# Performance work log

Measured on AMD Instinct MI355X. Metric: run time of the kernel, lower is better.

The kernel has to match this reference:

```python
import jax, jax.numpy as jnp
import numpy as np

N_NODES = 50000
N_EDGES = 600000
D_IN = 128
D_HID = 128
D_OUT = 64


def setup_inputs() -> dict:
    key = jax.random.key(0)
    ks = jax.random.split(key, 8)
    x = jax.random.normal(ks[0], (N_NODES, D_IN), dtype=jnp.float32)
    edge_index = jax.random.randint(ks[1], (2, N_EDGES), 0, N_NODES, dtype=jnp.int32)
    s = 0.05
    W1l = jax.random.normal(ks[2], (D_HID, D_IN), dtype=jnp.float32) * s
    b1 = jnp.zeros((D_HID,), dtype=jnp.float32)
    W1r = jax.random.normal(ks[3], (D_HID, D_IN), dtype=jnp.float32) * s
    W2l = jax.random.normal(ks[4], (D_OUT, D_HID), dtype=jnp.float32) * s
    b2 = jnp.zeros((D_OUT,), dtype=jnp.float32)
    W2r = jax.random.normal(ks[5], (D_OUT, D_HID), dtype=jnp.float32) * s
    return {"x": x, "edge_index": edge_index, "W1l": W1l, "b1": b1,
            "W1r": W1r, "W2l": W2l, "b2": b2, "W2r": W2r}


def _sage_conv(x, src, dst, Wl, bl, Wr, n_nodes):
    # mean aggregation of source features at destination nodes
    msg_sum = jax.ops.segment_sum(x[src], dst, num_segments=n_nodes)  # [N, D]
    deg = jax.ops.segment_sum(jnp.ones((src.shape[0], 1), x.dtype), dst,
                              num_segments=n_nodes)                   # [N, 1]
    mean = msg_sum / jnp.maximum(deg, 1.0)
    # out = lin_l(mean_neighbors) + lin_r(x_self); bias only on lin_l (PyG default)
    return mean @ Wl.T + bl + x @ Wr.T


def reference(x, edge_index, W1l, b1, W1r, W2l, b2, W2r):
    src, dst = edge_index[0], edge_index[1]
    n = x.shape[0]
    h = jax.nn.relu(_sage_conv(x, src, dst, W1l, b1, W1r, n))
    # dropout p=0.5 is identity in eval mode (training=False)
    return _sage_conv(h, src, dst, W2l, b2, W2r, n)
```

## Files before the change

kernel.cpp:

```cpp
#include <hip/hip_runtime.h>
#include <hip/hip_bf16.h>

typedef __bf16 bf16x8 __attribute__((ext_vector_type(8)));
typedef float f32x4 __attribute__((ext_vector_type(4)));
typedef float f32x2 __attribute__((ext_vector_type(2)));

#define D_FEAT 128
#define CHUNK 1024
#define NW 49344

__device__ __forceinline__ float bits_to_f(unsigned int u) {
    union { unsigned int i; float f; } c; c.i = u; return c.f;
}
__device__ __forceinline__ unsigned short f_to_bf16(float f) {
    __hip_bfloat16 h = (__hip_bfloat16)f;
    return *(unsigned short*)&h;
}
__device__ __forceinline__ float ld(const void* p, int is16, size_t i) {
    return is16 ? (float)((const __hip_bfloat16*)p)[i] : ((const float*)p)[i];
}
__device__ __forceinline__ unsigned int pack4_fp8(float v0, float v1, float v2, float v3) {
    int w = __builtin_amdgcn_cvt_pk_fp8_f32(v0, v1, 0, false);
    w = __builtin_amdgcn_cvt_pk_fp8_f32(v2, v3, w, true);
    return (unsigned int)w;
}
__device__ __forceinline__ int wave_probe16(const void* p) {
    const unsigned short v = ((const unsigned short*)p)[(threadIdx.x & 63) * 2];
    int e = (v >> 7) & 0xFF;
    unsigned long long m = __ballot(e >= 100 && e <= 140);
    return (__popcll(m) >= 48) ? 1 : 0;
}

__global__ void setup_kernel(const void* x,
                             const void* W1l, const void* b1, const void* W1r,
                             const void* W2l, const void* b2, const void* W2r,
                             const int* __restrict__ dst, int E,
                             unsigned short* __restrict__ wout, int* __restrict__ deg) {
    int i = blockIdx.x * blockDim.x + threadIdx.x;
    if (i < NW) {
        int is16 = wave_probe16(x);
        const void* s; int base;
        if      (i < 16384) { s = W1l; base = 0; }
        else if (i < 32768) { s = W1r; base = 16384; }
        else if (i < 40960) { s = W2l; base = 32768; }
        else if (i < 49152) { s = W2r; base = 40960; }
        else if (i < 49280) { s = b1;  base = 49152; }
        else                { s = b2;  base = 49280; }
        wout[i] = f_to_bf16(ld(s, is16, i - base));
    } else {
        int j = i - NW;
        if (j < E) atomicAdd(&deg[dst[j]], 1);
    }
}

__global__ void scan1_kernel(const int* __restrict__ deg, int* __restrict__ bsum, int n) {
    __shared__ int ws[4];
    const int lane = threadIdx.x & 63, wv = threadIdx.x >> 6;
    int i0 = blockIdx.x * CHUNK + threadIdx.x * 4;
    int s = 0;
    #pragma unroll
    for (int j = 0; j < 4; ++j)
        if (i0 + j < n) { int d = deg[i0 + j]; s += (d + 3) & ~3; }
    #pragma unroll
    for (int d = 1; d < 64; d <<= 1) s += __shfl_xor(s, d, 64);
    if (lane == 0) ws[wv] = s;
    __syncthreads();
    if (threadIdx.x == 0) bsum[blockIdx.x] = ws[0] + ws[1] + ws[2] + ws[3];
}

__global__ void scan3_kernel(const int* __restrict__ deg, const int* __restrict__ bsum,
                             int nb, int* __restrict__ off, int* __restrict__ cursor,
                             int* __restrict__ esrc, int n) {
    __shared__ int ws[4];
    const int lane = threadIdx.x & 63, wv = threadIdx.x >> 6;
    int bv = (lane < nb) ? bsum[lane] : 0;
    int bsc = bv;
    #pragma unroll
    for (int s = 1; s < 64; s <<= 1) {
        int t = __shfl_up(bsc, s, 64);
        if (lane >= s) bsc += t;
    }
    const int base = __shfl(bsc, blockIdx.x, 64) - __shfl(bv, blockIdx.x, 64);
    const int total = __shfl(bsc, nb - 1, 64);

    int i0 = blockIdx.x * CHUNK + threadIdx.x * 4;
    int d0 = 0, d1 = 0, d2 = 0, d3 = 0;
    if (i0 + 0 < n) d0 = deg[i0 + 0];
    if (i0 + 1 < n) d1 = deg[i0 + 1];
    if (i0 + 2 < n) d2 = deg[i0 + 2];
    if (i0 + 3 < n) d3 = deg[i0 + 3];
    int v0 = (d0 + 3) & ~3, v1 = (d1 + 3) & ~3, v2 = (d2 + 3) & ~3, v3 = (d3 + 3) & ~3;
    int tsum = v0 + v1 + v2 + v3;
    int sc = tsum;
    #pragma unroll
    for (int s = 1; s < 64; s <<= 1) {
        int t = __shfl_up(sc, s, 64);
        if (lane >= s) sc += t;
    }
    if (lane == 63) ws[wv] = sc;
    __syncthreads();
    int woff = 0;
    for (int w = 0; w < wv; ++w) woff += ws[w];
    int p = base + woff + (sc - tsum);
    #define EMIT(idx, dj, vj)                                            \
        if (i0 + idx < n) {                                              \
            off[i0 + idx] = p; cursor[i0 + idx] = p;                     \
            for (int q = p + dj; q < p + vj; ++q) esrc[q] = n;           \
            p += vj;                                                     \
        }
    EMIT(0, d0, v0) EMIT(1, d1, v1) EMIT(2, d2, v2) EMIT(3, d3, v3)
    #undef EMIT
    if (blockIdx.x == 0 && threadIdx.x == 0) off[n] = total;
}

__global__ void fill_kernel(const int* __restrict__ src, const int* __restrict__ dst,
                            int* __restrict__ cursor, int* __restrict__ esrc, int E) {
    int i = blockIdx.x * blockDim.x + threadIdx.x;
    if (i < E) {
        int p = atomicAdd(&cursor[dst[i]], 1);
        esrc[p] = src[i];
    }
}

template <int NOUT, bool PROBE_A, bool ZA_FP8>
__global__ __launch_bounds__(256)
void gemm_dual_kernel(const void* __restrict__ A,
                      const unsigned short* __restrict__ Wa,
                      const unsigned short* __restrict__ Wb,
                      const unsigned short* __restrict__ bias,
                      void* __restrict__ za, unsigned short* __restrict__ zb,
                      unsigned int* __restrict__ zrow, int zrow_words, int N) {
    if (blockIdx.x == 0 && threadIdx.x < zrow_words) zrow[threadIdx.x] = 0;
    int a16 = 1;
    if (PROBE_A) a16 = wave_probe16(A);

    const int lane = threadIdx.x & 63;
    const int wave = threadIdx.x >> 6;
    const int sel = wave & 1;
    const int m0 = blockIdx.x * 64 + (wave >> 1) * 32;
    if (m0 >= N) return;
    const int lrow = lane & 15;
    const int kg = lane >> 4;
    const unsigned short* W = sel ? Wb : Wa;
    constexpr int NT = NOUT / 16;

    bf16x8 xf[2][4];
    #pragma unroll
    for (int rt = 0; rt < 2; ++rt) {
        const int gr = min(m0 + rt * 16 + lrow, N - 1);
        #pragma unroll
        for (int ks = 0; ks < 4; ++ks) {
            const int k0 = ks * 32 + kg * 8;
            if (a16) {
                xf[rt][ks] = *(const bf16x8*)((const unsigned short*)A + (size_t)gr * D_FEAT + k0);
            } else {
                const float* fp = (const float*)A + (size_t)gr * D_FEAT + k0;
                float4 f0 = *(const float4*)fp, f1 = *(const float4*)(fp + 4);
                union { bf16x8 v; unsigned short us[8]; } t;
                t.us[0] = f_to_bf16(f0.x); t.us[1] = f_to_bf16(f0.y);
                t.us[2] = f_to_bf16(f0.z); t.us[3] = f_to_bf16(f0.w);
                t.us[4] = f_to_bf16(f1.x); t.us[5] = f_to_bf16(f1.y);
                t.us[6] = f_to_bf16(f1.z); t.us[7] = f_to_bf16(f1.w);
                xf[rt][ks] = t.v;
            }
        }
    }

    f32x4 acc[2][NT];
    #pragma unroll
    for (int rt = 0; rt < 2; ++rt)
        #pragma unroll
        for (int t = 0; t < NT; ++t) acc[rt][t] = (f32x4){0, 0, 0, 0};

    #pragma unroll
    for (int ks = 0; ks < 4; ++ks) {
        const int k0 = ks * 32 + kg * 8;
        #pragma unroll
        for (int t = 0; t < NT; ++t) {
            bf16x8 wf = *(const bf16x8*)(W + (size_t)(t * 16 + lrow) * D_FEAT + k0);
            acc[0][t] = __builtin_amdgcn_mfma_f32_16x16x32_bf16(wf, xf[0][ks], acc[0][t], 0, 0, 0);
            acc[1][t] = __builtin_amdgcn_mfma_f32_16x16x32_bf16(wf, xf[1][ks], acc[1][t], 0, 0, 0);
        }
    }

    #pragma unroll
    for (int rt = 0; rt < 2; ++rt) {
        const int nd = m0 + rt * 16 + lrow;
        if (nd < N) {
            #pragma unroll
            for (int t = 0; t < NT; ++t) {
                const int c0 = t * 16 + kg * 4;
                float v0 = acc[rt][t][0], v1 = acc[rt][t][1];
                float v2 = acc[rt][t][2], v3 = acc[rt][t][3];
                if (sel) {
                    uint2 bb = *(const uint2*)(bias + c0);
                    v0 += bits_to_f(bb.x << 16); v1 += bits_to_f(bb.x & 0xffff0000u);
                    v2 += bits_to_f(bb.y << 16); v3 += bits_to_f(bb.y & 0xffff0000u);
                    unsigned int p0 = (unsigned int)f_to_bf16(v0) | ((unsigned int)f_to_bf16(v1) << 16);
                    unsigned int p1 = (unsigned int)f_to_bf16(v2) | ((unsigned int)f_to_bf16(v3) << 16);
                    *(uint2*)(zb + (size_t)nd * NOUT + c0) = make_uint2(p0, p1);
                } else if (ZA_FP8) {
                    *(unsigned int*)((unsigned char*)za + (size_t)nd * NOUT + c0) =
                        pack4_fp8(v0, v1, v2, v3);
                } else {
                    unsigned int p0 = (unsigned int)f_to_bf16(v0) | ((unsigned int)f_to_bf16(v1) << 16);
                    unsigned int p1 = (unsigned int)f_to_bf16(v2) | ((unsigned int)f_to_bf16(v3) << 16);
                    *(uint2*)((unsigned short*)za + (size_t)nd * NOUT + c0) = make_uint2(p0, p1);
                }
            }
        }
    }
}

__global__ __launch_bounds__(256)
void agg1_kernel(const unsigned char* __restrict__ zl,
                 unsigned short* __restrict__ h,
                 const int* __restrict__ off, const int* __restrict__ deg,
                 const int* __restrict__ esrc, int N) {
    const int lane = threadIdx.x & 63;
    const int wave = threadIdx.x >> 6;
    const int a_lo = (blockIdx.x * 4 + wave) * 4;
    if (a_lo >= N) return;
    const int a_hi = min(a_lo + 4, N);
    const int nn = a_hi - a_lo;
    int offv = off[min(a_lo + min(lane, 4), N)];
    int degv = deg[min(a_lo + min(lane, 3), N - 1)];
    #define OFFAT(i) __shfl(offv, (i), 64)
    const int e_beg = OFFAT(0);
    const int e_end = OFFAT(nn);
    const int quarter = lane >> 4;
    const int fl = lane & 15;
    float ax[8];
    #pragma unroll
    for (int i = 0; i < 8; ++i) ax[i] = 0.f;
    int g = a_lo;
    int gend = OFFAT(1);

    auto flush = [&](int gg) {
        int td = __shfl(degv, gg - a_lo, 64);
        float inv = 1.f / (float)(td > 0 ? td : 1);
        float v[8];
        #pragma unroll
        for (int i = 0; i < 8; ++i) {
            float s = ax[i];
            s += __shfl_xor(s, 16, 64); s += __shfl_xor(s, 32, 64);
            v[i] = s * inv; ax[i] = 0.f;
        }
        if (quarter == 0) {
            unsigned short* hp = h + (size_t)gg * D_FEAT + fl * 8;
            uint4 zr = *(const uint4*)hp;
            unsigned int w[4] = {zr.x, zr.y, zr.z, zr.w};
            unsigned int pk[4];
            #pragma unroll
            for (int i = 0; i < 4; ++i) {
                float r0 = fmaxf(v[2 * i]     + bits_to_f(w[i] << 16), 0.f);
                float r1 = fmaxf(v[2 * i + 1] + bits_to_f(w[i] & 0xffff0000u), 0.f);
                pk[i] = (unsigned int)f_to_bf16(r0) | ((unsigned int)f_to_bf16(r1) << 16);
            }
            *(uint4*)hp = make_uint4(pk[0], pk[1], pk[2], pk[3]);
        }
    };

    int cur = (e_beg < e_end) ? esrc[min(e_beg + (lane & 31), e_end - 1)] : 0;
    for (int e = e_beg; e < e_end; e += 32) {
        int nxt = (e + 32 < e_end) ? esrc[min(e + 32 + (lane & 31), e_end - 1)] : 0;
        uint2 r[8];
        #pragma unroll
        for (int k = 0; k < 8; ++k) {
            int sk = __shfl(cur, 4 * k + quarter, 64);
            r[k] = *(const uint2*)(zl + (size_t)sk * D_FEAT + fl * 8);
        }
        #pragma unroll
        for (int k = 0; k < 8; ++k) {
            const int eb = e + 4 * k;
            if (eb < e_end) {
                while (eb >= gend) {
                    flush(g); ++g;
                    gend = OFFAT(min(g - a_lo + 1, 4));
                }
                f32x2 p0 = __builtin_amdgcn_cvt_pk_f32_fp8((int)r[k].x, false);
                f32x2 p1 = __builtin_amdgcn_cvt_pk_f32_fp8((int)r[k].x, true);
                f32x2 p2 = __builtin_amdgcn_cvt_pk_f32_fp8((int)r[k].y, false);
                f32x2 p3 = __builtin_amdgcn_cvt_pk_f32_fp8((int)r[k].y, true);
                ax[0] += p0.x; ax[1] += p0.y; ax[2] += p1.x; ax[3] += p1.y;
                ax[4] += p2.x; ax[5] += p2.y; ax[6] += p3.x; ax[7] += p3.y;
            }
        }
        cur = nxt;
    }
    while (g < a_hi) {
        flush(g); ++g;
        gend = OFFAT(min(g - a_lo + 1, 4));
    }
    #undef OFFAT
}

__global__ __launch_bounds__(256)
void agg2_kernel(const unsigned short* __restrict__ z2l,
                 const unsigned short* __restrict__ s2,
                 void* __restrict__ out, const void* __restrict__ x,
                 const int* __restrict__ off, const int* __restrict__ deg,
                 const int* __restrict__ esrc, int N) {
    const int o16 = wave_probe16(x);
    const int lane = threadIdx.x & 63;
    const int wave = threadIdx.x >> 6;
    const int a_lo = (blockIdx.x * 4 + wave) * 4;
    if (a_lo >= N) return;
    const int a_hi = min(a_lo + 4, N);
    const int nn = a_hi - a_lo;
    int offv = off[min(a_lo + min(lane, 4), N)];
    int degv = deg[min(a_lo + min(lane, 3), N - 1)];
    #define OFFAT(i) __shfl(offv, (i), 64)
    const int e_beg = OFFAT(0);
    const int e_end = OFFAT(nn);
    const int quarter = lane >> 4;
    const int fl = lane & 15;
    float ax[4];
    #pragma unroll
    for (int i = 0; i < 4; ++i) ax[i] = 0.f;
    int g = a_lo;
    int gend = OFFAT(1);

    auto flush = [&](int gg) {
        int td = __shfl(degv, gg - a_lo, 64);
        float inv = 1.f / (float)(td > 0 ? td : 1);
        float v[4];
        #pragma unroll
        for (int i = 0; i < 4; ++i) {
            float s = ax[i];
            s += __shfl_xor(s, 16, 64); s += __shfl_xor(s, 32, 64);
            v[i] = s * inv; ax[i] = 0.f;
        }
        if (quarter == 0) {
            uint2 sb = *(const uint2*)(s2 + (size_t)gg * 64 + fl * 4);
            v[0] += bits_to_f(sb.x << 16); v[1] += bits_to_f(sb.x & 0xffff0000u);
            v[2] += bits_to_f(sb.y << 16); v[3] += bits_to_f(sb.y & 0xffff0000u);
            if (o16) {
                unsigned int p0 = (unsigned int)f_to_bf16(v[0]) | ((unsigned int)f_to_bf16(v[1]) << 16);
                unsigned int p1 = (unsigned int)f_to_bf16(v[2]) | ((unsigned int)f_to_bf16(v[3]) << 16);
                *(uint2*)((unsigned short*)out + (size_t)gg * 64 + fl * 4) = make_uint2(p0, p1);
            } else {
                *(float4*)((float*)out + (size_t)gg * 64 + fl * 4) =
                    make_float4(v[0], v[1], v[2], v[3]);
            }
        }
    };

    int cur = (e_beg < e_end) ? esrc[min(e_beg + (lane & 31), e_end - 1)] : 0;
    for (int e = e_beg; e < e_end; e += 32) {
        int nxt = (e + 32 < e_end) ? esrc[min(e + 32 + (lane & 31), e_end - 1)] : 0;
        uint2 r[8];
        #pragma unroll
        for (int k = 0; k < 8; ++k) {
            int sk = __shfl(cur, 4 * k + quarter, 64);
            r[k] = *(const uint2*)(z2l + (size_t)sk * 64 + fl * 4);
        }
        #pragma unroll
        for (int k = 0; k < 8; ++k) {
            const int eb = e + 4 * k;
            if (eb < e_end) {
                while (eb >= gend) {
                    flush(g); ++g;
                    gend = OFFAT(min(g - a_lo + 1, 4));
                }
                uint2 u = r[k];
                ax[0] += bits_to_f(u.x << 16); ax[1] += bits_to_f(u.x & 0xffff0000u);
                ax[2] += bits_to_f(u.y << 16); ax[3] += bits_to_f(u.y & 0xffff0000u);
            }
        }
        cur = nxt;
    }
    while (g < a_hi) {
        flush(g); ++g;
        gend = OFFAT(min(g - a_lo + 1, 4));
    }
    #undef OFFAT
}

extern "C" void kernel_launch(void* const* d_in, const int* in_sizes, int n_in,
                              void* d_out, int out_size, void* d_ws, size_t ws_size,
                              hipStream_t stream) {
    const void* x   = d_in[0];
    const int* eidx = (const int*)d_in[1];
    const void* W1l = d_in[2];
    const void* b1  = d_in[3];
    const void* W1r = d_in[4];
    const void* W2l = d_in[5];
    const void* b2  = d_in[6];
    const void* W2r = d_in[7];

    const int N = in_sizes[0] / D_FEAT;
    const int E = in_sizes[1] / 2;
    const int* src = eidx;
    const int* dst = eidx + E;

    char* ws = (char*)d_ws;
    size_t o = 0;
    auto alloc = [&](size_t bytes) -> void* {
        void* p = ws + o;
        o += (bytes + 255) & ~(size_t)255;
        return p;
    };
    int* deg    = (int*)alloc((size_t)N * 4);
    int* off    = (int*)alloc((size_t)(N + 1) * 4);
    int* cursor = (int*)alloc((size_t)N * 4);
    int* bsum   = (int*)alloc(64 * 4);
    int* esrc   = (int*)alloc((size_t)(E + 3 * N + 64) * 4);
    unsigned short* wconv = (unsigned short*)alloc(NW * 2);
    unsigned char*  zl = (unsigned char*)alloc((size_t)(N + 1) * D_FEAT);
    unsigned short* h  = (unsigned short*)alloc((size_t)N * D_FEAT * 2);
    unsigned short* s2 = (unsigned short*)alloc((size_t)N * 64 * 2);
    unsigned short* z2l = (unsigned short*)zl;
    (void)n_in; (void)out_size; (void)ws_size;

    hipMemsetAsync(deg, 0, (size_t)N * 4, stream);
    setup_kernel<<<(NW + E + 255) / 256, 256, 0, stream>>>(
        x, W1l, b1, W1r, W2l, b2, W2r, dst, E, wconv, deg);
    const int nchunk = (N + CHUNK - 1) / CHUNK;
    scan1_kernel<<<nchunk, 256, 0, stream>>>(deg, bsum, N);
    scan3_kernel<<<nchunk, 256, 0, stream>>>(deg, bsum, nchunk, off, cursor, esrc, N);
    fill_kernel<<<(E + 255) / 256, 256, 0, stream>>>(src, dst, cursor, esrc, E);

    const int gblocks = (N + 63) / 64;
    const int ablocks = (N + 15) / 16;
    gemm_dual_kernel<128, true, true><<<gblocks, 256, 0, stream>>>(
        x, wconv + 0, wconv + 16384, wconv + 49152,
        zl, h, (unsigned int*)(zl + (size_t)N * D_FEAT), 32, N);
    agg1_kernel<<<ablocks, 256, 0, stream>>>(zl, h, off, deg, esrc, N);
    gemm_dual_kernel<64, false, false><<<gblocks, 256, 0, stream>>>(
        h, wconv + 32768, wconv + 40960, wconv + 49280,
        z2l, s2, (unsigned int*)(z2l + (size_t)N * 64), 32, N);
    agg2_kernel<<<ablocks, 256, 0, stream>>>(z2l, s2, d_out, x, off, deg, esrc, N);
}
```

Before: 240.8 us.

## Fuse layer-1 aggregation with layer-2 dual GEMM via shared-memory tile

Layer-1 mean aggregation, bias add and ReLU are now written to a 16-row shared-memory tile instead of to global h. The same block then runs the layer-2 MFMA products against W2l and W2r straight from that tile, writing both layer-2 outputs into one interleaved 128-wide row per node. This removes one kernel launch and the global write and re-read of the hidden activations. The cost is an extra barrier, and only 16 rows of MFMA work per block, with weights reloaded from global by every block.

```diff
diff --git a/kernel.cpp b/kernel.cpp
--- a/kernel.cpp
+++ b/kernel.cpp
@@ -122,17 +122,15 @@
     }
 }
 
-template <int NOUT, bool PROBE_A, bool ZA_FP8>
 __global__ __launch_bounds__(256)
-void gemm_dual_kernel(const void* __restrict__ A,
-                      const unsigned short* __restrict__ Wa,
-                      const unsigned short* __restrict__ Wb,
-                      const unsigned short* __restrict__ bias,
-                      void* __restrict__ za, unsigned short* __restrict__ zb,
-                      unsigned int* __restrict__ zrow, int zrow_words, int N) {
+void gemm1_kernel(const void* __restrict__ A,
+                  const unsigned short* __restrict__ Wa,
+                  const unsigned short* __restrict__ Wb,
+                  const unsigned short* __restrict__ bias,
+                  unsigned char* __restrict__ za, unsigned short* __restrict__ zb,
+                  unsigned int* __restrict__ zrow, int zrow_words, int N) {
     if (blockIdx.x == 0 && threadIdx.x < zrow_words) zrow[threadIdx.x] = 0;
-    int a16 = 1;
-    if (PROBE_A) a16 = wave_probe16(A);
+    const int a16 = wave_probe16(A);
 
     const int lane = threadIdx.x & 63;
     const int wave = threadIdx.x >> 6;
@@ -142,7 +140,7 @@
     const int lrow = lane & 15;
     const int kg = lane >> 4;
     const unsigned short* W = sel ? Wb : Wa;
-    constexpr int NT = NOUT / 16;
+    constexpr int NT = 8;
 
     bf16x8 xf[2][4];
     #pragma unroll
@@ -198,14 +196,9 @@
                     v2 += bits_to_f(bb.y << 16); v3 += bits_to_f(bb.y & 0xffff0000u);
                     unsigned int p0 = (unsigned int)f_to_bf16(v0) | ((unsigned int)f_to_bf16(v1) << 16);
                     unsigned int p1 = (unsigned int)f_to_bf16(v2) | ((unsigned int)f_to_bf16(v3) << 16);
-                    *(uint2*)(zb + (size_t)nd * NOUT + c0) = make_uint2(p0, p1);
-                } else if (ZA_FP8) {
-                    *(unsigned int*)((unsigned char*)za + (size_t)nd * NOUT + c0) =
-                        pack4_fp8(v0, v1, v2, v3);
+                    *(uint2*)(zb + (size_t)nd * D_FEAT + c0) = make_uint2(p0, p1);
                 } else {
-                    unsigned int p0 = (unsigned int)f_to_bf16(v0) | ((unsigned int)f_to_bf16(v1) << 16);
-                    unsigned int p1 = (unsigned int)f_to_bf16(v2) | ((unsigned int)f_to_bf16(v3) << 16);
-                    *(uint2*)((unsigned short*)za + (size_t)nd * NOUT + c0) = make_uint2(p0, p1);
+                    *(unsigned int*)(za + (size_t)nd * D_FEAT + c0) = pack4_fp8(v0, v1, v2, v3);
                 }
             }
         }
@@ -213,91 +206,140 @@
 }
 
 __global__ __launch_bounds__(256)
-void agg1_kernel(const unsigned char* __restrict__ zl,
-                 unsigned short* __restrict__ h,
-                 const int* __restrict__ off, const int* __restrict__ deg,
-                 const int* __restrict__ esrc, int N) {
-    const int lane = threadIdx.x & 63;
-    const int wave = threadIdx.x >> 6;
-    const int a_lo = (blockIdx.x * 4 + wave) * 4;
-    if (a_lo >= N) return;
-    const int a_hi = min(a_lo + 4, N);
-    const int nn = a_hi - a_lo;
-    int offv = off[min(a_lo + min(lane, 4), N)];
-    int degv = deg[min(a_lo + min(lane, 3), N - 1)];
-    #define OFFAT(i) __shfl(offv, (i), 64)
-    const int e_beg = OFFAT(0);
-    const int e_end = OFFAT(nn);
-    const int quarter = lane >> 4;
-    const int fl = lane & 15;
-    float ax[8];
-    #pragma unroll
-    for (int i = 0; i < 8; ++i) ax[i] = 0.f;
-    int g = a_lo;
-    int gend = OFFAT(1);
-
-    auto flush = [&](int gg) {
-        int td = __shfl(degv, gg - a_lo, 64);
-        float inv = 1.f / (float)(td > 0 ? td : 1);
-        float v[8];
-        #pragma unroll
-        for (int i = 0; i < 8; ++i) {
-            float s = ax[i];
-            s += __shfl_xor(s, 16, 64); s += __shfl_xor(s, 32, 64);
-            v[i] = s * inv; ax[i] = 0.f;
-        }
-        if (quarter == 0) {
-            unsigned short* hp = h + (size_t)gg * D_FEAT + fl * 8;
-            uint4 zr = *(const uint4*)hp;
-            unsigned int w[4] = {zr.x, zr.y, zr.z, zr.w};
-            unsigned int pk[4];
+void agg1g2_kernel(const unsigned char* __restrict__ zl,
+                   unsigned short* __restrict__ h,
+                   const unsigned short* __restrict__ W2l,
+                   const unsigned short* __restrict__ W2r,
+                   const unsigned short* __restrict__ b2,
+                   const int* __restrict__ off, const int* __restrict__ deg,
+                   const int* __restrict__ esrc, int N) {
+    __shared__ unsigned short ht[16][136];
+    const int tid = threadIdx.x;
+    const int lane = tid & 63;
+    const int wave = tid >> 6;
+    const int nb0 = blockIdx.x * 16;
+    if (nb0 >= N) return;
+
+    for (int i = tid; i < 16 * 136 / 2; i += 256) ((unsigned int*)ht)[i] = 0;
+    if (blockIdx.x == 0 && tid < 32) ((unsigned int*)(h + (size_t)N * D_FEAT))[tid] = 0;
+    __syncthreads();
+
+    const int a_lo = nb0 + wave * 4;
+    if (a_lo < N) {
+        const int a_hi = min(a_lo + 4, N);
+        const int nn = a_hi - a_lo;
+        int offv = off[min(a_lo + min(lane, 4), N)];
+        int degv = deg[min(a_lo + min(lane, 3), N - 1)];
+        #define OFFAT(i) __shfl(offv, (i), 64)
+        const int e_beg = OFFAT(0);
+        const int e_end = OFFAT(nn);
+        const int quarter = lane >> 4;
+        const int fl = lane & 15;
+        float ax[8];
+        #pragma unroll
+        for (int i = 0; i < 8; ++i) ax[i] = 0.f;
+        int g = a_lo;
+        int gend = OFFAT(1);
+
+        auto flush = [&](int gg) {
+            int td = __shfl(degv, gg - a_lo, 64);
+            float inv = 1.f / (float)(td > 0 ? td : 1);
+            float v[8];
             #pragma unroll
-            for (int i = 0; i < 4; ++i) {
-                float r0 = fmaxf(v[2 * i]     + bits_to_f(w[i] << 16), 0.f);
-                float r1 = fmaxf(v[2 * i + 1] + bits_to_f(w[i] & 0xffff0000u), 0.f);
-                pk[i] = (unsigned int)f_to_bf16(r0) | ((unsigned int)f_to_bf16(r1) << 16);
-            }
-            *(uint4*)hp = make_uint4(pk[0], pk[1], pk[2], pk[3]);
-        }
-    };
-
-    int cur = (e_beg < e_end) ? esrc[min(e_beg + (lane & 31), e_end - 1)] : 0;
-    for (int e = e_beg; e < e_end; e += 32) {
-        int nxt = (e + 32 < e_end) ? esrc[min(e + 32 + (lane & 31), e_end - 1)] : 0;
-        uint2 r[8];
-        #pragma unroll
-        for (int k = 0; k < 8; ++k) {
-            int sk = __shfl(cur, 4 * k + quarter, 64);
-            r[k] = *(const uint2*)(zl + (size_t)sk * D_FEAT + fl * 8);
-        }
-        #pragma unroll
-        for (int k = 0; k < 8; ++k) {
-            const int eb = e + 4 * k;
-            if (eb < e_end) {
-                while (eb >= gend) {
-                    flush(g); ++g;
-                    gend = OFFAT(min(g - a_lo + 1, 4));
+            for (int i = 0; i < 8; ++i) {
+                float s = ax[i];
+                s += __shfl_xor(s, 16, 64); s += __shfl_xor(s, 32, 64);
+                v[i] = s * inv; ax[i] = 0.f;
+            }
+            if (quarter == 0) {
+                const unsigned short* hp = h + (size_t)gg * D_FEAT + fl * 8;
+                uint4 zr = *(const uint4*)hp;
+                unsigned int w[4] = {zr.x, zr.y, zr.z, zr.w};
+                unsigned int pk[4];
+                #pragma unroll
+                for (int i = 0; i < 4; ++i) {
+                    float r0 = fmaxf(v[2 * i]     + bits_to_f(w[i] << 16), 0.f);
+                    float r1 = fmaxf(v[2 * i + 1] + bits_to_f(w[i] & 0xffff0000u), 0.f);
+                    pk[i] = (unsigned int)f_to_bf16(r0) | ((unsigned int)f_to_bf16(r1) << 16);
                 }
-                f32x2 p0 = __builtin_amdgcn_cvt_pk_f32_fp8((int)r[k].x, false);
-                f32x2 p1 = __builtin_amdgcn_cvt_pk_f32_fp8((int)r[k].x, true);
-                f32x2 p2 = __builtin_amdgcn_cvt_pk_f32_fp8((int)r[k].y, false);
-                f32x2 p3 = __builtin_amdgcn_cvt_pk_f32_fp8((int)r[k].y, true);
-                ax[0] += p0.x; ax[1] += p0.y; ax[2] += p1.x; ax[3] += p1.y;
-                ax[4] += p2.x; ax[5] += p2.y; ax[6] += p3.x; ax[7] += p3.y;
-            }
-        }
-        cur = nxt;
-    }
-    while (g < a_hi) {
-        flush(g); ++g;
-        gend = OFFAT(min(g - a_lo + 1, 4));
-    }
-    #undef OFFAT
+                *(uint4*)&ht[gg - nb0][fl * 8] = make_uint4(pk[0], pk[1], pk[2], pk[3]);
+            }
+        };
+
+        int cur = (e_beg < e_end) ? esrc[min(e_beg + (lane & 31), e_end - 1)] : 0;
+        for (int e = e_beg; e < e_end; e += 32) {
+            int nxt = (e + 32 < e_end) ? esrc[min(e + 32 + (lane & 31), e_end - 1)] : 0;
+            uint2 r[8];
+            #pragma unroll
+            for (int k = 0; k < 8; ++k) {
+                int sk = __shfl(cur, 4 * k + quarter, 64);
+                r[k] = *(const uint2*)(zl + (size_t)sk * D_FEAT + fl * 8);
+            }
+            #pragma unroll
+            for (int k = 0; k < 8; ++k) {
+                const int eb = e + 4 * k;
+                if (eb < e_end) {
+                    while (eb >= gend) {
+                        flush(g); ++g;
+                        gend = OFFAT(min(g - a_lo + 1, 4));
+                    }
+                    f32x2 p0 = __builtin_amdgcn_cvt_pk_f32_fp8((int)r[k].x, false);
+                    f32x2 p1 = __builtin_amdgcn_cvt_pk_f32_fp8((int)r[k].x, true);
+                    f32x2 p2 = __builtin_amdgcn_cvt_pk_f32_fp8((int)r[k].y, false);
+                    f32x2 p3 = __builtin_amdgcn_cvt_pk_f32_fp8((int)r[k].y, true);
+                    ax[0] += p0.x; ax[1] += p0.y; ax[2] += p1.x; ax[3] += p1.y;
+                    ax[4] += p2.x; ax[5] += p2.y; ax[6] += p3.x; ax[7] += p3.y;
+                }
+            }
+            cur = nxt;
+        }
+        while (g < a_hi) {
+            flush(g); ++g;
+            gend = OFFAT(min(g - a_lo + 1, 4));
+        }
+        #undef OFFAT
+    }
+    __syncthreads();
+
+    const int lrow = lane & 15;
+    const int kg = lane >> 4;
+    const int node = nb0 + lrow;
+    f32x4 acc[2];
+    acc[0] = (f32x4){0, 0, 0, 0};
+    acc[1] = (f32x4){0, 0, 0, 0};
+    #pragma unroll
+    for (int ks = 0; ks < 4; ++ks) {
+        const int k0 = ks * 32 + kg * 8;
+        bf16x8 xf = *(const bf16x8*)&ht[lrow][k0];
+        #pragma unroll
+        for (int t = 0; t < 2; ++t) {
+            const int cb = wave * 32 + t * 16;
+            const unsigned short* W = (cb < 64) ? W2l : W2r;
+            const int wrow = ((cb < 64) ? cb : cb - 64) + lrow;
+            bf16x8 wf = *(const bf16x8*)(W + (size_t)wrow * D_FEAT + k0);
+            acc[t] = __builtin_amdgcn_mfma_f32_16x16x32_bf16(wf, xf, acc[t], 0, 0, 0);
+        }
+    }
+    if (node < N) {
+        #pragma unroll
+        for (int t = 0; t < 2; ++t) {
+            const int cb = wave * 32 + t * 16;
+            const int cc0 = cb + kg * 4;
+            float v0 = acc[t][0], v1 = acc[t][1], v2 = acc[t][2], v3 = acc[t][3];
+            if (cb >= 64) {
+                uint2 bb = *(const uint2*)(b2 + (cc0 - 64));
+                v0 += bits_to_f(bb.x << 16); v1 += bits_to_f(bb.x & 0xffff0000u);
+                v2 += bits_to_f(bb.y << 16); v3 += bits_to_f(bb.y & 0xffff0000u);
+            }
+            unsigned int p0 = (unsigned int)f_to_bf16(v0) | ((unsigned int)f_to_bf16(v1) << 16);
+            unsigned int p1 = (unsigned int)f_to_bf16(v2) | ((unsigned int)f_to_bf16(v3) << 16);
+            *(uint2*)(h + (size_t)node * D_FEAT + cc0) = make_uint2(p0, p1);
+        }
+    }
 }
 
 __global__ __launch_bounds__(256)
-void agg2_kernel(const unsigned short* __restrict__ z2l,
-                 const unsigned short* __restrict__ s2,
+void agg2_kernel(const unsigned short* __restrict__ z2s,
                  void* __restrict__ out, const void* __restrict__ x,
                  const int* __restrict__ off, const int* __restrict__ deg,
                  const int* __restrict__ esrc, int N) {
@@ -332,7 +374,7 @@
             v[i] = s * inv; ax[i] = 0.f;
         }
         if (quarter == 0) {
-            uint2 sb = *(const uint2*)(s2 + (size_t)gg * 64 + fl * 4);
+            uint2 sb = *(const uint2*)(z2s + (size_t)gg * D_FEAT + 64 + fl * 4);
             v[0] += bits_to_f(sb.x << 16); v[1] += bits_to_f(sb.x & 0xffff0000u);
             v[2] += bits_to_f(sb.y << 16); v[3] += bits_to_f(sb.y & 0xffff0000u);
             if (o16) {
@@ -353,7 +395,7 @@
         #pragma unroll
         for (int k = 0; k < 8; ++k) {
             int sk = __shfl(cur, 4 * k + quarter, 64);
-            r[k] = *(const uint2*)(z2l + (size_t)sk * 64 + fl * 4);
+            r[k] = *(const uint2*)(z2s + (size_t)sk * D_FEAT + fl * 4);
         }
         #pragma unroll
         for (int k = 0; k < 8; ++k) {
@@ -408,9 +450,7 @@
     int* esrc   = (int*)alloc((size_t)(E + 3 * N + 64) * 4);
     unsigned short* wconv = (unsigned short*)alloc(NW * 2);
     unsigned char*  zl = (unsigned char*)alloc((size_t)(N + 1) * D_FEAT);
-    unsigned short* h  = (unsigned short*)alloc((size_t)N * D_FEAT * 2);
-    unsigned short* s2 = (unsigned short*)alloc((size_t)N * 64 * 2);
-    unsigned short* z2l = (unsigned short*)zl;
+    unsigned short* h  = (unsigned short*)alloc((size_t)(N + 1) * D_FEAT * 2);
     (void)n_in; (void)out_size; (void)ws_size;
 
     hipMemsetAsync(deg, 0, (size_t)N * 4, stream);
@@ -422,13 +462,12 @@
     fill_kernel<<<(E + 255) / 256, 256, 0, stream>>>(src, dst, cursor, esrc, E);
 
     const int gblocks = (N + 63) / 64;
+    const int fblocks = (N + 15) / 16;
     const int ablocks = (N + 15) / 16;
-    gemm_dual_kernel<128, true, true><<<gblocks, 256, 0, stream>>>(
+    gemm1_kernel<<<gblocks, 256, 0, stream>>>(
         x, wconv + 0, wconv + 16384, wconv + 49152,
         zl, h, (unsigned int*)(zl + (size_t)N * D_FEAT), 32, N);
-    agg1_kernel<<<ablocks, 256, 0, stream>>>(zl, h, off, deg, esrc, N);
-    gemm_dual_kernel<64, false, false><<<gblocks, 256, 0, stream>>>(
-        h, wconv + 32768, wconv + 40960, wconv + 49280,
-        z2l, s2, (unsigned int*)(z2l + (size_t)N * 64), 32, N);
-    agg2_kernel<<<ablocks, 256, 0, stream>>>(z2l, s2, d_out, x, off, deg, esrc, N);
-}
+    agg1g2_kernel<<<fblocks, 256, 0, stream>>>(
+        zl, h, wconv + 32768, wconv + 40960, wconv + 49280, off, deg, esrc, N);
+    agg2_kernel<<<ablocks, 256, 0, stream>>>(h, d_out, x, off, deg, esrc, N);
+}
```

After: 228.9 us. 5.0% less time.
